# Kernel tuning notes

Measured on AMD Instinct MI355X. Metric: run time of the kernel, lower is better.

Reference implementation:

```python
import jax, jax.numpy as jnp
import numpy as np

N_NODES = 100000
N_EDGES = 1600000
C_IN = 128
C_OUT = 128


def setup_inputs() -> dict:
    key = jax.random.key(0)
    k1, k2, k3, k4 = jax.random.split(key, 4)
    x = jax.random.normal(k1, (N_NODES, C_IN), dtype=jnp.float32)
    edge_index = jax.random.randint(k2, (2, N_EDGES), 0, N_NODES, dtype=jnp.int64)
    W = jax.random.normal(k3, (C_IN, C_OUT), dtype=jnp.float32) * (1.0 / np.sqrt(C_IN))
    b = jax.random.normal(k4, (C_OUT,), dtype=jnp.float32) * 0.01
    return {"x": x, "edge_index": edge_index, "W": W, "b": b}


def reference(x, edge_index, W, b):
    # EffSparseEdgeOnlyConv with aggr='add':
    #   x2  = lin2(x)
    #   deg = A @ ones         (per-destination-node edge count)
    #   out = A @ x2 - x2 * deg
    n = x.shape[0]
    dst = edge_index[0]  # COO row indices (aggregation target)
    src = edge_index[1]  # COO col indices (message source)
    x2 = x @ W + b  # [N, C_out]
    deg = jax.ops.segment_sum(
        jnp.ones((src.shape[0],), dtype=x.dtype), dst, num_segments=n
    )[:, None]  # [N, 1]
    agg = jax.ops.segment_sum(x2[src], dst, num_segments=n)  # [N, C_out]
    return agg - x2 * deg
```

## Files before the change

kernel.cpp:

```cpp
#include <hip/hip_runtime.h>


#define C_DIM 128
#define EPB 8192
#define MAXBK 1024

typedef __attribute__((ext_vector_type(8))) short bf16x8;
typedef __attribute__((ext_vector_type(4))) float f32x4;

__device__ __forceinline__ ushort f2b(float f) {
    uint u = __float_as_uint(f);
    u = (u + 0x7FFFu + ((u >> 16) & 1u)) >> 16;
    return (ushort)u;
}
__device__ __forceinline__ float b2f_lo(uint u) { return __uint_as_float(u << 16); }
__device__ __forceinline__ float b2f_hi(uint u) { return __uint_as_float(u & 0xFFFF0000u); }

__global__ __launch_bounds__(256) void gemm_mfma(const float* __restrict__ x,
                                                 const float* __restrict__ W,
                                                 float* __restrict__ x2f,
                                                 ushort* __restrict__ x2b,
                                                 int nrows) {
    __shared__ ushort Wt[128 * 128];
    const int tid = threadIdx.x;
    for (int i = tid; i < 4096; i += 256) {
        int k = i >> 5, n0 = (i & 31) * 4;
        float4 w = *(const float4*)(W + k * 128 + n0);
        float wv[4] = {w.x, w.y, w.z, w.w};
#pragma unroll
        for (int j = 0; j < 4; j++) {
            int n = n0 + j;
            Wt[(n * 128 + k) ^ ((n & 7) << 3)] = f2b(wv[j]);
        }
    }
    __syncthreads();

    const int wv_ = tid >> 6;
    const int lane = tid & 63;
    const int ln = lane & 15, kg = lane >> 4;
    const int row_base = blockIdx.x * 128 + wv_ * 32;

    f32x4 acc[2][8];
#pragma unroll
    for (int a = 0; a < 2; a++)
#pragma unroll
        for (int b = 0; b < 8; b++) acc[a][b] = (f32x4)(0.f);

#pragma unroll
    for (int step = 0; step < 4; step++) {
        const int k0 = step * 32 + kg * 8;
        bf16x8 bfr[8];
#pragma unroll
        for (int cf = 0; cf < 8; cf++) {
            int n = cf * 16 + ln;
            bfr[cf] = *(const bf16x8*)&Wt[(n * 128 + k0) ^ ((n & 7) << 3)];
        }
#pragma unroll
        for (int mf = 0; mf < 2; mf++) {
            int row = row_base + mf * 16 + ln;
            bf16x8 afr;
#pragma unroll
            for (int j = 0; j < 8; j++) afr[j] = 0;
            if (row < nrows) {
                const float4* ap = (const float4*)(x + (size_t)row * 128 + k0);
                float4 a0 = ap[0], a1 = ap[1];
                float av[8] = {a0.x, a0.y, a0.z, a0.w, a1.x, a1.y, a1.z, a1.w};
#pragma unroll
                for (int j = 0; j < 8; j++) afr[j] = (short)f2b(av[j]);
            }
#pragma unroll
            for (int cf = 0; cf < 8; cf++)
                acc[mf][cf] = __builtin_amdgcn_mfma_f32_16x16x32_bf16(afr, bfr[cf], acc[mf][cf], 0, 0, 0);
        }
    }

#pragma unroll
    for (int mf = 0; mf < 2; mf++) {
#pragma unroll
        for (int j = 0; j < 4; j++) {
            int row = row_base + mf * 16 + kg * 4 + j;
            if (row >= nrows) continue;
#pragma unroll
            for (int cf = 0; cf < 8; cf++) {
                float v = acc[mf][cf][j];
                int col = cf * 16 + ln;
                x2f[(size_t)row * 128 + col] = v;
                if (x2b) x2b[(size_t)row * 128 + col] = f2b(v);
            }
        }
    }
}

__global__ __launch_bounds__(256) void zero_ints(int* p, int n) {
    int i = blockIdx.x * 256 + threadIdx.x;
    if (i < n) p[i] = 0;
}

__global__ __launch_bounds__(256) void bucket_hist(const int* __restrict__ ei,
                                                   int* __restrict__ bcnt,
                                                   int ne, int nn, int nbk) {
    __shared__ int hist[MAXBK];
    const int e0 = blockIdx.x * EPB;
    const int e1 = min(ne, e0 + EPB);
    for (int i = threadIdx.x; i < nbk; i += 256) hist[i] = 0;
    __syncthreads();
    for (int e = e0 + threadIdx.x; e < e1; e += 256) {
        int dst = ei[e];
        if ((unsigned)dst < (unsigned)nn) atomicAdd(&hist[dst >> 7], 1);
    }
    __syncthreads();
    for (int i = threadIdx.x; i < nbk; i += 256) {
        int h = hist[i];
        if (h > 0) atomicAdd(&bcnt[i], h);
    }
}

__global__ __launch_bounds__(1024) void bucket_scan(const int* __restrict__ bcnt,
                                                    int* __restrict__ bstart,
                                                    int* __restrict__ bnext, int nbk) {
    __shared__ int s[1024];
    int v = (threadIdx.x < nbk) ? bcnt[threadIdx.x] : 0;
    s[threadIdx.x] = v;
    __syncthreads();
    for (int off = 1; off < 1024; off <<= 1) {
        int t = (threadIdx.x >= off) ? s[threadIdx.x - off] : 0;
        __syncthreads();
        s[threadIdx.x] += t;
        __syncthreads();
    }
    if (threadIdx.x < nbk) {
        bstart[threadIdx.x] = s[threadIdx.x] - v;
        bnext[threadIdx.x] = 0;
        if (threadIdx.x == nbk - 1) bstart[nbk] = s[threadIdx.x];
    }
}

__global__ __launch_bounds__(256) void bin_edges2(const int* __restrict__ ei,
                                                  const int* __restrict__ bstart,
                                                  int* __restrict__ bnext,
                                                  uint* __restrict__ bbuf,
                                                  int ne, int nn, int nbk) {
    __shared__ int hist[MAXBK];
    __shared__ int base[MAXBK];
    const int e0 = blockIdx.x * EPB;
    const int e1 = min(ne, e0 + EPB);
    for (int i = threadIdx.x; i < nbk; i += 256) hist[i] = 0;
    __syncthreads();
    for (int e = e0 + threadIdx.x; e < e1; e += 256) {
        int dst = ei[e];
        if ((unsigned)dst < (unsigned)nn) atomicAdd(&hist[dst >> 7], 1);
    }
    __syncthreads();
    for (int i = threadIdx.x; i < nbk; i += 256) {
        int h = hist[i];
        int b0 = (h > 0) ? atomicAdd(&bnext[i], h) : 0;
        base[i] = bstart[i] + b0;
        hist[i] = 0;
    }
    __syncthreads();
    for (int e = e0 + threadIdx.x; e < e1; e += 256) {
        int dst = ei[e];
        int src = ei[ne + e];
        if ((unsigned)dst >= (unsigned)nn || (unsigned)src >= (unsigned)nn) continue;
        int b = dst >> 7;
        int r = atomicAdd(&hist[b], 1);
        bbuf[base[b] + r] = ((uint)(dst & 127) << 17) | (uint)src;
    }
}

__global__ __launch_bounds__(256) void sort_bucket2(const uint* __restrict__ bbuf,
                                                    const int* __restrict__ bstart,
                                                    int* __restrict__ csr,
                                                    int* __restrict__ start,
                                                    int* __restrict__ cnt, int n) {
    __shared__ int h[128];
    __shared__ int sb[128];
    const int b = blockIdx.x;
    const int d0 = b << 7;
    const int base = bstart[b];
    const int end = bstart[b + 1];
    if (threadIdx.x < 128) h[threadIdx.x] = 0;
    __syncthreads();
    for (int i = base + threadIdx.x; i < end; i += 256)
        atomicAdd(&h[bbuf[i] >> 17], 1);
    __syncthreads();
    if (threadIdx.x < 128) sb[threadIdx.x] = h[threadIdx.x];
    __syncthreads();
    for (int off = 1; off < 128; off <<= 1) {
        int t = 0;
        if (threadIdx.x < 128 && threadIdx.x >= off) t = sb[threadIdx.x - off];
        __syncthreads();
        if (threadIdx.x < 128) sb[threadIdx.x] += t;
        __syncthreads();
    }
    if (threadIdx.x < 128) {
        int excl = sb[threadIdx.x] - h[threadIdx.x];
        int gbase = base + excl;
        sb[threadIdx.x] = gbase;
        int d = d0 + threadIdx.x;
        if (d < n) { start[d] = gbase; cnt[d] = h[threadIdx.x]; }
        h[threadIdx.x] = 0;
    }
    __syncthreads();
    for (int i = base + threadIdx.x; i < end; i += 256) {
        uint p = bbuf[i];
        int d7 = (int)(p >> 17);
        int src = (int)(p & 0x1FFFFu);
        int r = atomicAdd(&h[d7], 1);
        csr[sb[d7] + r] = src;
    }
}

__global__ __launch_bounds__(256) void count_deg(const int* __restrict__ ei,
                                                 int* __restrict__ cnt, int ne, int nn) {
    int e = blockIdx.x * 256 + threadIdx.x;
    if (e >= ne) return;
    int dst = ei[e];
    if ((unsigned)dst < (unsigned)nn) atomicAdd(&cnt[dst], 1);
}

__global__ __launch_bounds__(256) void scan_partials(const int* __restrict__ cnt,
                                                     int* __restrict__ bsum, int n) {
    __shared__ int red[256];
    int i = blockIdx.x * 1024 + threadIdx.x * 4;
    int s = 0;
    if (i + 3 < n) {
        int4 v = *(const int4*)(cnt + i);
        s = v.x + v.y + v.z + v.w;
    } else {
        for (int j = i; j < n && j < i + 4; j++) s += cnt[j];
    }
    red[threadIdx.x] = s;
    __syncthreads();
    for (int off = 128; off > 0; off >>= 1) {
        if (threadIdx.x < off) red[threadIdx.x] += red[threadIdx.x + off];
        __syncthreads();
    }
    if (threadIdx.x == 0) bsum[blockIdx.x] = red[0];
}

__global__ __launch_bounds__(1024) void scan_bsums(int* __restrict__ bsum, int nb) {
    __shared__ int s[1024];
    int v = (threadIdx.x < nb) ? bsum[threadIdx.x] : 0;
    s[threadIdx.x] = v;
    __syncthreads();
    for (int off = 1; off < 1024; off <<= 1) {
        int t = (threadIdx.x >= off) ? s[threadIdx.x - off] : 0;
        __syncthreads();
        s[threadIdx.x] += t;
        __syncthreads();
    }
    if (threadIdx.x < nb) bsum[threadIdx.x] = s[threadIdx.x] - v;
}

__global__ __launch_bounds__(256) void scan_apply(const int* __restrict__ cnt,
                                                  const int* __restrict__ bsum,
                                                  int* __restrict__ start,
                                                  int* __restrict__ next, int n) {
    __shared__ int s[256];
    int i = blockIdx.x * 1024 + threadIdx.x * 4;
    int4 v = make_int4(0, 0, 0, 0);
    if (i + 3 < n) {
        v = *(const int4*)(cnt + i);
    } else {
        if (i + 0 < n) v.x = cnt[i + 0];
        if (i + 1 < n) v.y = cnt[i + 1];
        if (i + 2 < n) v.z = cnt[i + 2];
        if (i + 3 < n) v.w = cnt[i + 3];
    }
    int tsum = v.x + v.y + v.z + v.w;
    s[threadIdx.x] = tsum;
    __syncthreads();
    for (int off = 1; off < 256; off <<= 1) {
        int t = (threadIdx.x >= off) ? s[threadIdx.x - off] : 0;
        __syncthreads();
        s[threadIdx.x] += t;
        __syncthreads();
    }
    int r0 = s[threadIdx.x] - tsum + bsum[blockIdx.x];
    int r1 = r0 + v.x, r2 = r1 + v.y, r3 = r2 + v.z;
    if (i + 3 < n) {
        *(int4*)(start + i) = make_int4(r0, r1, r2, r3);
        *(int4*)(next + i) = make_int4(r0, r1, r2, r3);
    } else {
        int rr[4] = {r0, r1, r2, r3};
        for (int j = 0; j < 4 && i + j < n; j++) {
            start[i + j] = rr[j];
            next[i + j] = rr[j];
        }
    }
}

__global__ __launch_bounds__(256) void fill_csr(const int* __restrict__ ei,
                                                int* __restrict__ next,
                                                int* __restrict__ csr, int ne, int nn) {
    int e = blockIdx.x * 256 + threadIdx.x;
    if (e >= ne) return;
    int dst = ei[e];
    int src = ei[ne + e];
    if ((unsigned)dst >= (unsigned)nn || (unsigned)src >= (unsigned)nn) return;
    int slot = atomicAdd(&next[dst], 1);
    csr[slot] = src;
}

__global__ __launch_bounds__(256) void gather_b16(const int* __restrict__ csr,
                                                  const int* __restrict__ start,
                                                  const int* __restrict__ cnt,
                                                  const uint* __restrict__ x2b,
                                                  const float* __restrict__ x2f,
                                                  float* __restrict__ out, int nn) {
    int wave = (int)((blockIdx.x * 256 + threadIdx.x) >> 6);
    int lane = threadIdx.x & 63;
    if (wave >= nn) return;
    const int s0 = start[wave];
    const int dg = cnt[wave];
    float a0 = 0, a1 = 0, b0 = 0, b1 = 0, c0 = 0, c1 = 0, d0 = 0, d1 = 0;
    int e = 0;
    for (; e + 4 <= dg; e += 4) {
        int s1 = csr[s0 + e], s2 = csr[s0 + e + 1];
        int s3 = csr[s0 + e + 2], s4 = csr[s0 + e + 3];
        uint u1 = x2b[(size_t)s1 * 64 + lane];
        uint u2 = x2b[(size_t)s2 * 64 + lane];
        uint u3 = x2b[(size_t)s3 * 64 + lane];
        uint u4 = x2b[(size_t)s4 * 64 + lane];
        a0 += b2f_lo(u1); a1 += b2f_hi(u1);
        b0 += b2f_lo(u2); b1 += b2f_hi(u2);
        c0 += b2f_lo(u3); c1 += b2f_hi(u3);
        d0 += b2f_lo(u4); d1 += b2f_hi(u4);
    }
    for (; e < dg; e++) {
        int s1 = csr[s0 + e];
        uint u1 = x2b[(size_t)s1 * 64 + lane];
        a0 += b2f_lo(u1); a1 += b2f_hi(u1);
    }
    float2 self = ((const float2*)(x2f + (size_t)wave * 128))[lane];
    float d = (float)dg;
    float2 o;
    o.x = (a0 + b0) + (c0 + d0) - d * self.x;
    o.y = (a1 + b1) + (c1 + d1) - d * self.y;
    ((float2*)out)[(size_t)wave * 64 + lane] = o;
}

__global__ __launch_bounds__(256) void gather_out(const int* __restrict__ csr,
                                                  const int* __restrict__ start,
                                                  const int* __restrict__ cnt,
                                                  const float* __restrict__ x2,
                                                  float* __restrict__ out, int nn) {
    int wave = (int)((blockIdx.x * 256 + threadIdx.x) >> 6);
    int lane = threadIdx.x & 63;
    if (wave >= nn) return;
    const int s0 = start[wave];
    const int dg = cnt[wave];
    const float2* __restrict__ base = (const float2*)x2;
    float2 acc0 = make_float2(0.f, 0.f), acc1 = make_float2(0.f, 0.f);
    int e = 0;
    for (; e + 2 <= dg; e += 2) {
        int s1 = csr[s0 + e], s2 = csr[s0 + e + 1];
        float2 v1 = base[(size_t)s1 * 64 + lane];
        float2 v2 = base[(size_t)s2 * 64 + lane];
        acc0.x += v1.x; acc0.y += v1.y;
        acc1.x += v2.x; acc1.y += v2.y;
    }
    if (e < dg) {
        int s1 = csr[s0 + e];
        float2 v1 = base[(size_t)s1 * 64 + lane];
        acc0.x += v1.x; acc0.y += v1.y;
    }
    float2 self = base[(size_t)wave * 64 + lane];
    float d = (float)dg;
    float2 o;
    o.x = acc0.x + acc1.x - d * self.x;
    o.y = acc0.y + acc1.y - d * self.y;
    ((float2*)out)[(size_t)wave * 64 + lane] = o;
}

extern "C" void kernel_launch(void* const* d_in, const int* in_sizes, int n_in,
                              void* d_out, int out_size, void* d_ws, size_t ws_size,
                              hipStream_t stream) {
    const float* x = (const float*)d_in[0];
    const int* ei = (const int*)d_in[1];
    const float* W = (const float*)d_in[2];
    float* out = (float*)d_out;

    const int n = in_sizes[0] / C_DIM;
    const int ne = in_sizes[1] / 2;
    const int nbk = (n + 127) / 128;
    const int nb = (n + 1023) / 1024;

    const size_t sz_x2f = (size_t)n * C_DIM * sizeof(float);
    const size_t sz_x2b = (size_t)n * C_DIM * sizeof(ushort);
    const size_t sz_int = (size_t)n * sizeof(int);
    const size_t sz_bkt = (size_t)((nbk + 4) & ~3) * sizeof(int);
    const size_t sz_e = (size_t)ne * sizeof(int);
    const size_t sz_bs = (size_t)((nb + 3) & ~3) * sizeof(int);
    const size_t need_bin = sz_x2f + sz_x2b + 2 * sz_int + 3 * sz_bkt + 2 * sz_e;
    const size_t need_b16 = sz_x2f + sz_x2b + 3 * sz_int + sz_bs + sz_e;
    const bool use_bin = ws_size >= need_bin && nbk <= MAXBK && n < (1 << 17);
    const bool use_b16 = use_bin || ws_size >= need_b16;

    char* ws = (char*)d_ws;
    float* x2f = (float*)ws;                ws += sz_x2f;
    ushort* x2b = nullptr;
    if (use_b16) { x2b = (ushort*)ws;       ws += sz_x2b; }
    int* cnt = (int*)ws;                    ws += sz_int;
    int* start = (int*)ws;                  ws += sz_int;
    int *csr = nullptr, *next = nullptr, *bsum = nullptr;
    int *bcnt = nullptr, *bstart = nullptr, *bnext = nullptr;
    uint* bbuf = nullptr;

    if (use_bin) {
        bcnt = (int*)ws;                    ws += sz_bkt;
        bstart = (int*)ws;                  ws += sz_bkt;
        bnext = (int*)ws;                   ws += sz_bkt;
        csr = (int*)ws;                     ws += sz_e;
        bbuf = (uint*)ws;
    } else {
        bsum = (int*)ws;                    ws += sz_bs;
        next = (int*)ws;                    ws += sz_int;
        csr = (int*)ws;
    }

    int ntiles = (n + 127) / 128;
    int binblocks = (ne + EPB - 1) / EPB;
    int eblocks = (ne + 255) / 256;

    if (use_bin) {
        zero_ints<<<(nbk + 255) / 256, 256, 0, stream>>>(bcnt, nbk);

        gemm_mfma<<<ntiles, 256, 0, stream>>>(x, W, x2f, x2b, n);

        bucket_hist<<<binblocks, 256, 0, stream>>>(ei, bcnt, ne, n, nbk);
        bucket_scan<<<1, 1024, 0, stream>>>(bcnt, bstart, bnext, nbk);
        bin_edges2<<<binblocks, 256, 0, stream>>>(ei, bstart, bnext, bbuf, ne, n, nbk);
        sort_bucket2<<<nbk, 256, 0, stream>>>(bbuf, bstart, csr, start, cnt, n);
    } else {
        zero_ints<<<(n + 255) / 256, 256, 0, stream>>>(cnt, n);
        gemm_mfma<<<ntiles, 256, 0, stream>>>(x, W, x2f, x2b, n);
        count_deg<<<eblocks, 256, 0, stream>>>(ei, cnt, ne, n);
        scan_partials<<<nb, 256, 0, stream>>>(cnt, bsum, n);
        scan_bsums<<<1, 1024, 0, stream>>>(bsum, nb);
        scan_apply<<<nb, 256, 0, stream>>>(cnt, bsum, start, next, n);
        fill_csr<<<eblocks, 256, 0, stream>>>(ei, next, csr, ne, n);
    }

    int gblocks = (n + 3) / 4;
    if (use_b16)
        gather_b16<<<gblocks, 256, 0, stream>>>(csr, start, cnt, (const uint*)x2b, x2f, out, n);
    else
        gather_out<<<gblocks, 256, 0, stream>>>(csr, start, cnt, x2f, out, n);
}
```

Before: 280.4 us.

## Drop fp32 x2 copy, use per-block bucket offsets instead of atomics

The binned path no longer writes the fp32 copy of x2. The gather now reads the self term from the bf16 buffer, which removes 51 MB of GEMM writes and a strided self read. Bucket binning now stores a per-block histogram matrix and column-scans it, so bin_edges no longer recomputes the histogram or uses global atomics for offsets. It also drops the zero_ints launch. The cost is reduced precision on the self term (bf16) and an extra small column-scan kernel whose serial loop runs over about 196 blocks.

```diff
diff --git a/kernel.cpp b/kernel.cpp
--- a/kernel.cpp
+++ b/kernel.cpp
@@ -84,7 +84,7 @@
             for (int cf = 0; cf < 8; cf++) {
                 float v = acc[mf][cf][j];
                 int col = cf * 16 + ln;
-                x2f[(size_t)row * 128 + col] = v;
+                if (x2f) x2f[(size_t)row * 128 + col] = v;
                 if (x2b) x2b[(size_t)row * 128 + col] = f2b(v);
             }
         }
@@ -96,9 +96,9 @@
     if (i < n) p[i] = 0;
 }
 
-__global__ __launch_bounds__(256) void bucket_hist(const int* __restrict__ ei,
-                                                   int* __restrict__ bcnt,
-                                                   int ne, int nn, int nbk) {
+__global__ __launch_bounds__(256) void bucket_hist2(const int* __restrict__ ei,
+                                                    int* __restrict__ gbh,
+                                                    int ne, int nn, int nbk) {
     __shared__ int hist[MAXBK];
     const int e0 = blockIdx.x * EPB;
     const int e1 = min(ne, e0 + EPB);
@@ -109,17 +109,29 @@
         if ((unsigned)dst < (unsigned)nn) atomicAdd(&hist[dst >> 7], 1);
     }
     __syncthreads();
-    for (int i = threadIdx.x; i < nbk; i += 256) {
-        int h = hist[i];
-        if (h > 0) atomicAdd(&bcnt[i], h);
-    }
-}
-
-__global__ __launch_bounds__(1024) void bucket_scan(const int* __restrict__ bcnt,
-                                                    int* __restrict__ bstart,
-                                                    int* __restrict__ bnext, int nbk) {
+    int* row = gbh + (size_t)blockIdx.x * nbk;
+    for (int i = threadIdx.x; i < nbk; i += 256) row[i] = hist[i];
+}
+
+__global__ __launch_bounds__(256) void bucket_colscan(int* __restrict__ gbh,
+                                                      int* __restrict__ tot,
+                                                      int nbk, int nblk) {
+    int i = blockIdx.x * 256 + threadIdx.x;
+    if (i >= nbk) return;
+    int run = 0;
+    for (int b = 0; b < nblk; b++) {
+        size_t idx = (size_t)b * nbk + i;
+        int v = gbh[idx];
+        gbh[idx] = run;
+        run += v;
+    }
+    tot[i] = run;
+}
+
+__global__ __launch_bounds__(1024) void bucket_scan(const int* __restrict__ tot,
+                                                    int* __restrict__ bstart, int nbk) {
     __shared__ int s[1024];
-    int v = (threadIdx.x < nbk) ? bcnt[threadIdx.x] : 0;
+    int v = (threadIdx.x < nbk) ? tot[threadIdx.x] : 0;
     s[threadIdx.x] = v;
     __syncthreads();
     for (int off = 1; off < 1024; off <<= 1) {
@@ -130,32 +142,23 @@
     }
     if (threadIdx.x < nbk) {
         bstart[threadIdx.x] = s[threadIdx.x] - v;
-        bnext[threadIdx.x] = 0;
         if (threadIdx.x == nbk - 1) bstart[nbk] = s[threadIdx.x];
     }
 }
 
-__global__ __launch_bounds__(256) void bin_edges2(const int* __restrict__ ei,
+__global__ __launch_bounds__(256) void bin_edges3(const int* __restrict__ ei,
                                                   const int* __restrict__ bstart,
-                                                  int* __restrict__ bnext,
+                                                  const int* __restrict__ gbh,
                                                   uint* __restrict__ bbuf,
                                                   int ne, int nn, int nbk) {
-    __shared__ int hist[MAXBK];
     __shared__ int base[MAXBK];
+    __shared__ int h[MAXBK];
     const int e0 = blockIdx.x * EPB;
     const int e1 = min(ne, e0 + EPB);
-    for (int i = threadIdx.x; i < nbk; i += 256) hist[i] = 0;
-    __syncthreads();
-    for (int e = e0 + threadIdx.x; e < e1; e += 256) {
-        int dst = ei[e];
-        if ((unsigned)dst < (unsigned)nn) atomicAdd(&hist[dst >> 7], 1);
-    }
-    __syncthreads();
+    const int* row = gbh + (size_t)blockIdx.x * nbk;
     for (int i = threadIdx.x; i < nbk; i += 256) {
-        int h = hist[i];
-        int b0 = (h > 0) ? atomicAdd(&bnext[i], h) : 0;
-        base[i] = bstart[i] + b0;
-        hist[i] = 0;
+        base[i] = bstart[i] + row[i];
+        h[i] = 0;
     }
     __syncthreads();
     for (int e = e0 + threadIdx.x; e < e1; e += 256) {
@@ -163,7 +166,7 @@
         int src = ei[ne + e];
         if ((unsigned)dst >= (unsigned)nn || (unsigned)src >= (unsigned)nn) continue;
         int b = dst >> 7;
-        int r = atomicAdd(&hist[b], 1);
+        int r = atomicAdd(&h[b], 1);
         bbuf[base[b] + r] = ((uint)(dst & 127) << 17) | (uint)src;
     }
 }
@@ -211,104 +214,11 @@
     }
 }
 
-__global__ __launch_bounds__(256) void count_deg(const int* __restrict__ ei,
-                                                 int* __restrict__ cnt, int ne, int nn) {
-    int e = blockIdx.x * 256 + threadIdx.x;
-    if (e >= ne) return;
-    int dst = ei[e];
-    if ((unsigned)dst < (unsigned)nn) atomicAdd(&cnt[dst], 1);
-}
-
-__global__ __launch_bounds__(256) void scan_partials(const int* __restrict__ cnt,
-                                                     int* __restrict__ bsum, int n) {
-    __shared__ int red[256];
-    int i = blockIdx.x * 1024 + threadIdx.x * 4;
-    int s = 0;
-    if (i + 3 < n) {
-        int4 v = *(const int4*)(cnt + i);
-        s = v.x + v.y + v.z + v.w;
-    } else {
-        for (int j = i; j < n && j < i + 4; j++) s += cnt[j];
-    }
-    red[threadIdx.x] = s;
-    __syncthreads();
-    for (int off = 128; off > 0; off >>= 1) {
-        if (threadIdx.x < off) red[threadIdx.x] += red[threadIdx.x + off];
-        __syncthreads();
-    }
-    if (threadIdx.x == 0) bsum[blockIdx.x] = red[0];
-}
-
-__global__ __launch_bounds__(1024) void scan_bsums(int* __restrict__ bsum, int nb) {
-    __shared__ int s[1024];
-    int v = (threadIdx.x < nb) ? bsum[threadIdx.x] : 0;
-    s[threadIdx.x] = v;
-    __syncthreads();
-    for (int off = 1; off < 1024; off <<= 1) {
-        int t = (threadIdx.x >= off) ? s[threadIdx.x - off] : 0;
-        __syncthreads();
-        s[threadIdx.x] += t;
-        __syncthreads();
-    }
-    if (threadIdx.x < nb) bsum[threadIdx.x] = s[threadIdx.x] - v;
-}
-
-__global__ __launch_bounds__(256) void scan_apply(const int* __restrict__ cnt,
-                                                  const int* __restrict__ bsum,
-                                                  int* __restrict__ start,
-                                                  int* __restrict__ next, int n) {
-    __shared__ int s[256];
-    int i = blockIdx.x * 1024 + threadIdx.x * 4;
-    int4 v = make_int4(0, 0, 0, 0);
-    if (i + 3 < n) {
-        v = *(const int4*)(cnt + i);
-    } else {
-        if (i + 0 < n) v.x = cnt[i + 0];
-        if (i + 1 < n) v.y = cnt[i + 1];
-        if (i + 2 < n) v.z = cnt[i + 2];
-        if (i + 3 < n) v.w = cnt[i + 3];
-    }
-    int tsum = v.x + v.y + v.z + v.w;
-    s[threadIdx.x] = tsum;
-    __syncthreads();
-    for (int off = 1; off < 256; off <<= 1) {
-        int t = (threadIdx.x >= off) ? s[threadIdx.x - off] : 0;
-        __syncthreads();
-        s[threadIdx.x] += t;
-        __syncthreads();
-    }
-    int r0 = s[threadIdx.x] - tsum + bsum[blockIdx.x];
-    int r1 = r0 + v.x, r2 = r1 + v.y, r3 = r2 + v.z;
-    if (i + 3 < n) {
-        *(int4*)(start + i) = make_int4(r0, r1, r2, r3);
-        *(int4*)(next + i) = make_int4(r0, r1, r2, r3);
-    } else {
-        int rr[4] = {r0, r1, r2, r3};
-        for (int j = 0; j < 4 && i + j < n; j++) {
-            start[i + j] = rr[j];
-            next[i + j] = rr[j];
-        }
-    }
-}
-
-__global__ __launch_bounds__(256) void fill_csr(const int* __restrict__ ei,
-                                                int* __restrict__ next,
-                                                int* __restrict__ csr, int ne, int nn) {
-    int e = blockIdx.x * 256 + threadIdx.x;
-    if (e >= ne) return;
-    int dst = ei[e];
-    int src = ei[ne + e];
-    if ((unsigned)dst >= (unsigned)nn || (unsigned)src >= (unsigned)nn) return;
-    int slot = atomicAdd(&next[dst], 1);
-    csr[slot] = src;
-}
-
-__global__ __launch_bounds__(256) void gather_b16(const int* __restrict__ csr,
-                                                  const int* __restrict__ start,
-                                                  const int* __restrict__ cnt,
-                                                  const uint* __restrict__ x2b,
-                                                  const float* __restrict__ x2f,
-                                                  float* __restrict__ out, int nn) {
+__global__ __launch_bounds__(256) void gather_b16b(const int* __restrict__ csr,
+                                                   const int* __restrict__ start,
+                                                   const int* __restrict__ cnt,
+                                                   const uint* __restrict__ x2b,
+                                                   float* __restrict__ out, int nn) {
     int wave = (int)((blockIdx.x * 256 + threadIdx.x) >> 6);
     int lane = threadIdx.x & 63;
     if (wave >= nn) return;
@@ -333,12 +243,104 @@
         uint u1 = x2b[(size_t)s1 * 64 + lane];
         a0 += b2f_lo(u1); a1 += b2f_hi(u1);
     }
-    float2 self = ((const float2*)(x2f + (size_t)wave * 128))[lane];
+    uint us = x2b[(size_t)wave * 64 + lane];
     float d = (float)dg;
     float2 o;
-    o.x = (a0 + b0) + (c0 + d0) - d * self.x;
-    o.y = (a1 + b1) + (c1 + d1) - d * self.y;
+    o.x = (a0 + b0) + (c0 + d0) - d * b2f_lo(us);
+    o.y = (a1 + b1) + (c1 + d1) - d * b2f_hi(us);
     ((float2*)out)[(size_t)wave * 64 + lane] = o;
+}
+
+__global__ __launch_bounds__(256) void count_deg(const int* __restrict__ ei,
+                                                 int* __restrict__ cnt, int ne, int nn) {
+    int e = blockIdx.x * 256 + threadIdx.x;
+    if (e >= ne) return;
+    int dst = ei[e];
+    if ((unsigned)dst < (unsigned)nn) atomicAdd(&cnt[dst], 1);
+}
+
+__global__ __launch_bounds__(256) void scan_partials(const int* __restrict__ cnt,
+                                                     int* __restrict__ bsum, int n) {
+    __shared__ int red[256];
+    int i = blockIdx.x * 1024 + threadIdx.x * 4;
+    int s = 0;
+    if (i + 3 < n) {
+        int4 v = *(const int4*)(cnt + i);
+        s = v.x + v.y + v.z + v.w;
+    } else {
+        for (int j = i; j < n && j < i + 4; j++) s += cnt[j];
+    }
+    red[threadIdx.x] = s;
+    __syncthreads();
+    for (int off = 128; off > 0; off >>= 1) {
+        if (threadIdx.x < off) red[threadIdx.x] += red[threadIdx.x + off];
+        __syncthreads();
+    }
+    if (threadIdx.x == 0) bsum[blockIdx.x] = red[0];
+}
+
+__global__ __launch_bounds__(1024) void scan_bsums(int* __restrict__ bsum, int nb) {
+    __shared__ int s[1024];
+    int v = (threadIdx.x < nb) ? bsum[threadIdx.x] : 0;
+    s[threadIdx.x] = v;
+    __syncthreads();
+    for (int off = 1; off < 1024; off <<= 1) {
+        int t = (threadIdx.x >= off) ? s[threadIdx.x - off] : 0;
+        __syncthreads();
+        s[threadIdx.x] += t;
+        __syncthreads();
+    }
+    if (threadIdx.x < nb) bsum[threadIdx.x] = s[threadIdx.x] - v;
+}
+
+__global__ __launch_bounds__(256) void scan_apply(const int* __restrict__ cnt,
+                                                  const int* __restrict__ bsum,
+                                                  int* __restrict__ start,
+                                                  int* __restrict__ next, int n) {
+    __shared__ int s[256];
+    int i = blockIdx.x * 1024 + threadIdx.x * 4;
+    int4 v = make_int4(0, 0, 0, 0);
+    if (i + 3 < n) {
+        v = *(const int4*)(cnt + i);
+    } else {
+        if (i + 0 < n) v.x = cnt[i + 0];
+        if (i + 1 < n) v.y = cnt[i + 1];
+        if (i + 2 < n) v.z = cnt[i + 2];
+        if (i + 3 < n) v.w = cnt[i + 3];
+    }
+    int tsum = v.x + v.y + v.z + v.w;
+    s[threadIdx.x] = tsum;
+    __syncthreads();
+    for (int off = 1; off < 256; off <<= 1) {
+        int t = (threadIdx.x >= off) ? s[threadIdx.x - off] : 0;
+        __syncthreads();
+        s[threadIdx.x] += t;
+        __syncthreads();
+    }
+    int r0 = s[threadIdx.x] - tsum + bsum[blockIdx.x];
+    int r1 = r0 + v.x, r2 = r1 + v.y, r3 = r2 + v.z;
+    if (i + 3 < n) {
+        *(int4*)(start + i) = make_int4(r0, r1, r2, r3);
+        *(int4*)(next + i) = make_int4(r0, r1, r2, r3);
+    } else {
+        int rr[4] = {r0, r1, r2, r3};
+        for (int j = 0; j < 4 && i + j < n; j++) {
+            start[i + j] = rr[j];
+            next[i + j] = rr[j];
+        }
+    }
+}
+
+__global__ __launch_bounds__(256) void fill_csr(const int* __restrict__ ei,
+                                                int* __restrict__ next,
+                                                int* __restrict__ csr, int ne, int nn) {
+    int e = blockIdx.x * 256 + threadIdx.x;
+    if (e >= ne) return;
+    int dst = ei[e];
+    int src = ei[ne + e];
+    if ((unsigned)dst >= (unsigned)nn || (unsigned)src >= (unsigned)nn) return;
+    int slot = atomicAdd(&next[dst], 1);
+    csr[slot] = src;
 }
 
 __global__ __launch_bounds__(256) void gather_out(const int* __restrict__ csr,
@@ -386,66 +388,61 @@
     const int ne = in_sizes[1] / 2;
     const int nbk = (n + 127) / 128;
     const int nb = (n + 1023) / 1024;
+    const int binblocks = (ne + EPB - 1) / EPB;
 
     const size_t sz_x2f = (size_t)n * C_DIM * sizeof(float);
     const size_t sz_x2b = (size_t)n * C_DIM * sizeof(ushort);
     const size_t sz_int = (size_t)n * sizeof(int);
     const size_t sz_bkt = (size_t)((nbk + 4) & ~3) * sizeof(int);
+    const size_t sz_gbh = (size_t)binblocks * nbk * sizeof(int);
     const size_t sz_e = (size_t)ne * sizeof(int);
     const size_t sz_bs = (size_t)((nb + 3) & ~3) * sizeof(int);
-    const size_t need_bin = sz_x2f + sz_x2b + 2 * sz_int + 3 * sz_bkt + 2 * sz_e;
-    const size_t need_b16 = sz_x2f + sz_x2b + 3 * sz_int + sz_bs + sz_e;
+    const size_t need_bin = sz_x2b + 2 * sz_int + 2 * sz_bkt + sz_gbh + 2 * sz_e;
+    const size_t need_f32 = sz_x2f + 3 * sz_int + sz_bs + sz_e;
     const bool use_bin = ws_size >= need_bin && nbk <= MAXBK && n < (1 << 17);
-    const bool use_b16 = use_bin || ws_size >= need_b16;
 
     char* ws = (char*)d_ws;
-    float* x2f = (float*)ws;                ws += sz_x2f;
-    ushort* x2b = nullptr;
-    if (use_b16) { x2b = (ushort*)ws;       ws += sz_x2b; }
-    int* cnt = (int*)ws;                    ws += sz_int;
-    int* start = (int*)ws;                  ws += sz_int;
-    int *csr = nullptr, *next = nullptr, *bsum = nullptr;
-    int *bcnt = nullptr, *bstart = nullptr, *bnext = nullptr;
-    uint* bbuf = nullptr;
 
     if (use_bin) {
-        bcnt = (int*)ws;                    ws += sz_bkt;
-        bstart = (int*)ws;                  ws += sz_bkt;
-        bnext = (int*)ws;                   ws += sz_bkt;
-        csr = (int*)ws;                     ws += sz_e;
-        bbuf = (uint*)ws;
+        ushort* x2b = (ushort*)ws;          ws += sz_x2b;
+        int* cnt = (int*)ws;                ws += sz_int;
+        int* start = (int*)ws;              ws += sz_int;
+        int* bstart = (int*)ws;             ws += sz_bkt;
+        int* tot = (int*)ws;                ws += sz_bkt;
+        int* gbh = (int*)ws;                ws += sz_gbh;
+        int* csr = (int*)ws;                ws += sz_e;
+        uint* bbuf = (uint*)ws;
+
+        int ntiles = (n + 127) / 128;
+        gemm_mfma<<<ntiles, 256, 0, stream>>>(x, W, nullptr, x2b, n);
+
+        bucket_hist2<<<binblocks, 256, 0, stream>>>(ei, gbh, ne, n, nbk);
+        bucket_colscan<<<(nbk + 255) / 256, 256, 0, stream>>>(gbh, tot, nbk, binblocks);
+        bucket_scan<<<1, 1024, 0, stream>>>(tot, bstart, nbk);
+        bin_edges3<<<binblocks, 256, 0, stream>>>(ei, bstart, gbh, bbuf, ne, n, nbk);
+        sort_bucket2<<<nbk, 256, 0, stream>>>(bbuf, bstart, csr, start, cnt, n);
+
+        int gblocks = (n + 3) / 4;
+        gather_b16b<<<gblocks, 256, 0, stream>>>(csr, start, cnt, (const uint*)x2b, out, n);
     } else {
-        bsum = (int*)ws;                    ws += sz_bs;
-        next = (int*)ws;                    ws += sz_int;
-        csr = (int*)ws;
-    }
-
-    int ntiles = (n + 127) / 128;
-    int binblocks = (ne + EPB - 1) / EPB;
-    int eblocks = (ne + 255) / 256;
-
-    if (use_bin) {
-        zero_ints<<<(nbk + 255) / 256, 256, 0, stream>>>(bcnt, nbk);
-
-        gemm_mfma<<<ntiles, 256, 0, stream>>>(x, W, x2f, x2b, n);
-
-        bucket_hist<<<binblocks, 256, 0, stream>>>(ei, bcnt, ne, n, nbk);
-        bucket_scan<<<1, 1024, 0, stream>>>(bcnt, bstart, bnext, nbk);
-        bin_edges2<<<binblocks, 256, 0, stream>>>(ei, bstart, bnext, bbuf, ne, n, nbk);
-        sort_bucket2<<<nbk, 256, 0, stream>>>(bbuf, bstart, csr, start, cnt, n);
-    } else {
+        float* x2f = (float*)ws;            ws += sz_x2f;
+        int* cnt = (int*)ws;                ws += sz_int;
+        int* start = (int*)ws;              ws += sz_int;
+        int* bsum = (int*)ws;               ws += sz_bs;
+        int* next = (int*)ws;               ws += sz_int;
+        int* csr = (int*)ws;
+        (void)need_f32;
+
         zero_ints<<<(n + 255) / 256, 256, 0, stream>>>(cnt, n);
-        gemm_mfma<<<ntiles, 256, 0, stream>>>(x, W, x2f, x2b, n);
+        int ntiles = (n + 127) / 128;
+        gemm_mfma<<<ntiles, 256, 0, stream>>>(x, W, x2f, nullptr, n);
+        int eblocks = (ne + 255) / 256;
         count_deg<<<eblocks, 256, 0, stream>>>(ei, cnt, ne, n);
         scan_partials<<<nb, 256, 0, stream>>>(cnt, bsum, n);
         scan_bsums<<<1, 1024, 0, stream>>>(bsum, nb);
         scan_apply<<<nb, 256, 0, stream>>>(cnt, bsum, start, next, n);
         fill_csr<<<eblocks, 256, 0, stream>>>(ei, next, csr, ne, n);
-    }
-
-    int gblocks = (n + 3) / 4;
-    if (use_b16)
-        gather_b16<<<gblocks, 256, 0, stream>>>(csr, start, cnt, (const uint*)x2b, x2f, out, n);
-    else
+        int gblocks = (n + 3) / 4;
         gather_out<<<gblocks, 256, 0, stream>>>(csr, start, cnt, x2f, out, n);
-}
+    }
+}
```

Measured after the change: 306.9 us. 9.4% more time.
